# Performance work log

Measured on AMD Instinct MI355X. Metric: run time of the kernel, lower is better.

Reference implementation:

```python
import jax, jax.numpy as jnp
import numpy as np

N_NODES = 100000
N_EDGES = 1600000
EDGES_IN = 1
HID = 64
OUT = 64


def setup_inputs() -> dict:
    key = jax.random.key(0)
    ks = jax.random.split(key, 10)
    s = lambda fan_in: 1.0 / np.sqrt(fan_in)
    inp = {
        "edge_index": jax.random.randint(ks[0], (2, N_EDGES), 0, N_NODES, dtype=jnp.int64) if jax.config.jax_enable_x64 else jax.random.randint(ks[0], (2, N_EDGES), 0, N_NODES, dtype=jnp.int32),
        "edge_attr": jax.random.normal(ks[1], (N_EDGES, EDGES_IN), dtype=jnp.float32),
        # edge MLP: Linear(EDGES_IN->HID), SiLU, Linear(HID->HID), SiLU
        "W1": jax.random.uniform(ks[2], (EDGES_IN, HID), jnp.float32, -s(EDGES_IN), s(EDGES_IN)),
        "b1": jax.random.uniform(ks[3], (HID,), jnp.float32, -s(EDGES_IN), s(EDGES_IN)),
        "W2": jax.random.uniform(ks[4], (HID, HID), jnp.float32, -s(HID), s(HID)),
        "b2": jax.random.uniform(ks[5], (HID,), jnp.float32, -s(HID), s(HID)),
        # node MLP: Linear(HID->HID), SiLU, Linear(HID->OUT)
        "W3": jax.random.uniform(ks[6], (HID, HID), jnp.float32, -s(HID), s(HID)),
        "b3": jax.random.uniform(ks[7], (HID,), jnp.float32, -s(HID), s(HID)),
        "W4": jax.random.uniform(ks[8], (HID, OUT), jnp.float32, -s(HID), s(HID)),
        "b4": jax.random.uniform(ks[9], (OUT,), jnp.float32, -s(HID), s(HID)),
    }
    return inp


def reference(edge_index, edge_attr, W1, b1, W2, b2, W3, b3, W4, b4):
    silu = jax.nn.silu
    # edge model: [E, EDGES_IN] -> [E, HID]
    ef = silu(edge_attr @ W1 + b1)
    ef = silu(ef @ W2 + b2)
    # unsorted_segment_sum over source nodes (row): [E, HID] -> [N, HID]
    row = edge_index[0]
    agg = jax.ops.segment_sum(ef, row, num_segments=N_NODES)
    # node model: [N, HID] -> [N, OUT]
    h = silu(agg @ W3 + b3) @ W4 + b4
    return h
```

## Files before the change

kernel.cpp:

```cpp
#include <hip/hip_runtime.h>
#include <math.h>
#include <utility>

#define TN 4096
#define XMIN (-8.0f)
#define XMAX (8.0f)

#define GB1 256
#define MAXBK 4096
#define BKN 32
#define BKCAP 1024

typedef __attribute__((ext_vector_type(8))) short short8;
typedef __attribute__((ext_vector_type(4))) float f32x4;
typedef __attribute__((ext_vector_type(4))) int   int4v;
typedef __attribute__((ext_vector_type(4))) float f4v;

__device__ __forceinline__ float silu_f(float v) {
    return v / (1.0f + __expf(-v));
}

__device__ __forceinline__ unsigned short f2bf(float x) {
    unsigned u = __float_as_uint(x);
    return (unsigned short)((u + 0x7FFFu + ((u >> 16) & 1u)) >> 16);
}
__device__ __forceinline__ float bf2f(unsigned short h) {
    return __uint_as_float(((unsigned)h) << 16);
}

#define SPLIT8(w0,w1,w2,w3,w4,w5,w6,w7, H, L) { \
    unsigned short _h0=f2bf(w0),_h1=f2bf(w1),_h2=f2bf(w2),_h3=f2bf(w3), \
                   _h4=f2bf(w4),_h5=f2bf(w5),_h6=f2bf(w6),_h7=f2bf(w7); \
    H = (short8){(short)_h0,(short)_h1,(short)_h2,(short)_h3, \
                 (short)_h4,(short)_h5,(short)_h6,(short)_h7}; \
    L = (short8){(short)f2bf((w0)-bf2f(_h0)),(short)f2bf((w1)-bf2f(_h1)), \
                 (short)f2bf((w2)-bf2f(_h2)),(short)f2bf((w3)-bf2f(_h3)), \
                 (short)f2bf((w4)-bf2f(_h4)),(short)f2bf((w5)-bf2f(_h5)), \
                 (short)f2bf((w6)-bf2f(_h6)),(short)f2bf((w7)-bf2f(_h7))}; }

#define BFRAG(Wp, kc, nt, H, L) { \
    const float* _p = (Wp) + ((kc)*32 + quad*8)*64 + (nt)*16 + m; \
    SPLIT8(_p[0],_p[64],_p[128],_p[192],_p[256],_p[320],_p[384],_p[448], H, L) }

#define MFMA3(AH, AL, BH, BL, ACC) \
    ACC = __builtin_amdgcn_mfma_f32_16x16x32_bf16(AH, BH, ACC, 0, 0, 0); \
    ACC = __builtin_amdgcn_mfma_f32_16x16x32_bf16(AL, BH, ACC, 0, 0, 0); \
    ACC = __builtin_amdgcn_mfma_f32_16x16x32_bf16(AH, BL, ACC, 0, 0, 0);

__global__ void build_table_k(const float* __restrict__ W1, const float* __restrict__ b1,
                              const float* __restrict__ W2, const float* __restrict__ b2,
                              float* __restrict__ table2, int* __restrict__ cnt, int nbk) {
    int gid  = blockIdx.x * blockDim.x + threadIdx.x;
    if (gid < nbk) cnt[gid] = 0;
    int wave = gid >> 6;
    int lane = gid & 63;
    if (wave >= TN) return;
    const float step = (XMAX - XMIN) / (float)(TN - 1);
    float x  = XMIN + step * (float)wave;
    float h1 = silu_f(fmaf(x, W1[lane], b1[lane]));
    float acc = b2[lane];
#pragma unroll
    for (int k = 0; k < 64; ++k) {
        float h1k = __shfl(h1, k, 64);
        acc = fmaf(h1k, W2[k * 64 + lane], acc);
    }
    float val = silu_f(acc);
    table2[(size_t)wave * 128 + 2 * lane] = val;
    if (wave > 0)
        table2[(size_t)(wave - 1) * 128 + 2 * lane + 1] = val;
}

__global__ void pack_w_k(const float* __restrict__ W3, const float* __restrict__ W4,
                         short8* __restrict__ packW) {
    int t = threadIdx.x, lane = t & 63, wid = t >> 6;
    int m = lane & 15, quad = lane >> 4;
    for (int f = wid; f < 16; f += 4) {
        const float* Wp = (f < 8) ? W3 : W4;
        int kc = f & 1, nt = (f >> 1) & 3;
        short8 H, L;
        BFRAG(Wp, kc, nt, H, L)
        packW[(2 * f + 0) * 64 + lane] = H;
        packW[(2 * f + 1) * 64 + lane] = L;
    }
}

__global__ void bscatter_k(const int* __restrict__ row, const float* __restrict__ x,
                           int* __restrict__ cnt, unsigned int* __restrict__ packed,
                           int E, int nbk) {
    __shared__ int hist[MAXBK];
    int t = threadIdx.x;
    for (int e = t; e < nbk; e += 256) hist[e] = 0;
    __syncthreads();
    int E4 = E >> 2;
    for (int i4 = blockIdx.x * 256 + t; i4 < E4; i4 += 256 * GB1) {
        int4v r4 = ((const int4v*)row)[i4];
        atomicAdd(&hist[r4[0] >> 5], 1);
        atomicAdd(&hist[r4[1] >> 5], 1);
        atomicAdd(&hist[r4[2] >> 5], 1);
        atomicAdd(&hist[r4[3] >> 5], 1);
    }
    if (blockIdx.x == 0)
        for (int i = (E4 << 2) + t; i < E; i += 256)
            atomicAdd(&hist[row[i] >> 5], 1);
    __syncthreads();
    int shift = (int)(((long)blockIdx.x * nbk) >> 8);
    for (int k = t; k < nbk; k += 256) {
        int e = k + shift; if (e >= nbk) e -= nbk;
        int c = hist[e];
        hist[e] = c ? (e * BKCAP + atomicAdd(&cnt[e], c)) : 0;
    }
    __syncthreads();
    const float scale = (float)(TN - 1) / (XMAX - XMIN);
    for (int i4 = blockIdx.x * 256 + t; i4 < E4; i4 += 256 * GB1) {
        int4v r4 = ((const int4v*)row)[i4];
        f4v   x4 = ((const f4v*)x)[i4];
#pragma unroll
        for (int k = 0; k < 4; ++k) {
            int r = r4[k];
            float tt = fminf(fmaxf((x4[k] - XMIN) * scale, 0.f), (float)(TN - 1) - 0.001f);
            int   i0 = (int)tt;
            unsigned int q = min((unsigned int)((tt - (float)i0) * 8192.0f), 8191u);
            unsigned int pk = ((unsigned int)(r & 31) << 25) | ((unsigned int)i0 << 13) | q;
            int bk = r >> 5;
            int p = atomicAdd(&hist[bk], 1);
            if (p < (bk + 1) * BKCAP) packed[p] = pk;
        }
    }
    if (blockIdx.x == 0) {
        for (int i = (E4 << 2) + t; i < E; i += 256) {
            int r = row[i];
            float xv = x[i];
            float tt = fminf(fmaxf((xv - XMIN) * scale, 0.f), (float)(TN - 1) - 0.001f);
            int   i0 = (int)tt;
            unsigned int q = min((unsigned int)((tt - (float)i0) * 8192.0f), 8191u);
            unsigned int pk = ((unsigned int)(r & 31) << 25) | ((unsigned int)i0 << 13) | q;
            int bk = r >> 5;
            int p = atomicAdd(&hist[bk], 1);
            if (p < (bk + 1) * BKCAP) packed[p] = pk;
        }
    }
}

__global__ __launch_bounds__(256, 8)
void gather_k(const unsigned int* __restrict__ packed, const int* __restrict__ cntArr,
              const float* __restrict__ table2, float* __restrict__ aggOut, int N) {
    __shared__ __align__(16) unsigned int srt[BKCAP];
    __shared__ int hist[BKN + 1];
    __shared__ int curs[BKN];
    int t = threadIdx.x, lane = t & 63, wid = t >> 6;
    int b = blockIdx.x;

    int s   = b * BKCAP;
    int cnt = min(cntArr[b], BKCAP);

    if (t <= BKN) hist[t] = 0;
    __syncthreads();

    uint4 myq;
    int mybase = t << 2;
    int myrem = 0;
    if (mybase < cnt) {
        myq = *(const uint4*)&packed[s + mybase];
        myrem = cnt - mybase; if (myrem > 4) myrem = 4;
        if (myrem > 0) atomicAdd(&hist[myq.x >> 25], 1);
        if (myrem > 1) atomicAdd(&hist[myq.y >> 25], 1);
        if (myrem > 2) atomicAdd(&hist[myq.z >> 25], 1);
        if (myrem > 3) atomicAdd(&hist[myq.w >> 25], 1);
    }
    __syncthreads();

    if (wid == 0 && lane < BKN) {
        int c = hist[lane];
        int sc = c;
#pragma unroll
        for (int d = 1; d < BKN; d <<= 1) {
            int u = __shfl_up(sc, d, 64);
            if (lane >= d) sc += u;
        }
        hist[lane] = sc - c;  curs[lane] = sc - c;
        if (lane == BKN - 1) hist[BKN] = sc;
    }
    __syncthreads();

    if (myrem > 0) { int p = atomicAdd(&curs[myq.x >> 25], 1); srt[p] = myq.x; }
    if (myrem > 1) { int p = atomicAdd(&curs[myq.y >> 25], 1); srt[p] = myq.y; }
    if (myrem > 2) { int p = atomicAdd(&curs[myq.z >> 25], 1); srt[p] = myq.z; }
    if (myrem > 3) { int p = atomicAdd(&curs[myq.w >> 25], 1); srt[p] = myq.w; }
    __syncthreads();

    const float2* tb = (const float2*)table2;
#define EDGE_UV(sp, uv, f) \
    const float2* _rp = tb + (((sp >> 13) & 0xFFFu) << 6); \
    float2 uv = _rp[lane]; \
    float f = (float)(sp & 0x1FFFu) * (1.0f / 8192.0f);

    for (int nl = wid; nl < BKN; nl += 4) {
        int n = (b << 5) + nl;
        if (n >= N) break;
        int beg = hist[nl], dn = hist[nl + 1] - beg;
        float a0 = 0.f, a1 = 0.f, a2 = 0.f, a3 = 0.f;
        int j = 0;
        int head = (4 - (beg & 3)) & 3;
        if (head > dn) head = dn;
        for (; j < head; ++j) {
            unsigned sp0 = (unsigned)__builtin_amdgcn_readfirstlane(srt[beg + j]);
            EDGE_UV(sp0, uv0, f0)
            a0 = fmaf(f0, uv0.y - uv0.x, a0 + uv0.x);
        }
        for (; j + 8 <= dn; j += 8) {
            uint4 qa = *(const uint4*)&srt[beg + j];
            uint4 qb = *(const uint4*)&srt[beg + j + 4];
            unsigned sp0 = (unsigned)__builtin_amdgcn_readfirstlane(qa.x);
            unsigned sp1 = (unsigned)__builtin_amdgcn_readfirstlane(qa.y);
            unsigned sp2 = (unsigned)__builtin_amdgcn_readfirstlane(qa.z);
            unsigned sp3 = (unsigned)__builtin_amdgcn_readfirstlane(qa.w);
            unsigned sp4 = (unsigned)__builtin_amdgcn_readfirstlane(qb.x);
            unsigned sp5 = (unsigned)__builtin_amdgcn_readfirstlane(qb.y);
            unsigned sp6 = (unsigned)__builtin_amdgcn_readfirstlane(qb.z);
            unsigned sp7 = (unsigned)__builtin_amdgcn_readfirstlane(qb.w);
            { EDGE_UV(sp0, uv0, f0) a0 = fmaf(f0, uv0.y - uv0.x, a0 + uv0.x); }
            { EDGE_UV(sp1, uv1, f1) a1 = fmaf(f1, uv1.y - uv1.x, a1 + uv1.x); }
            { EDGE_UV(sp2, uv2, f2) a2 = fmaf(f2, uv2.y - uv2.x, a2 + uv2.x); }
            { EDGE_UV(sp3, uv3, f3) a3 = fmaf(f3, uv3.y - uv3.x, a3 + uv3.x); }
            { EDGE_UV(sp4, uv4, f4) a0 = fmaf(f4, uv4.y - uv4.x, a0 + uv4.x); }
            { EDGE_UV(sp5, uv5, f5) a1 = fmaf(f5, uv5.y - uv5.x, a1 + uv5.x); }
            { EDGE_UV(sp6, uv6, f6) a2 = fmaf(f6, uv6.y - uv6.x, a2 + uv6.x); }
            { EDGE_UV(sp7, uv7, f7) a3 = fmaf(f7, uv7.y - uv7.x, a3 + uv7.x); }
        }
        for (; j + 4 <= dn; j += 4) {
            uint4 q = *(const uint4*)&srt[beg + j];
            unsigned sp0 = (unsigned)__builtin_amdgcn_readfirstlane(q.x);
            unsigned sp1 = (unsigned)__builtin_amdgcn_readfirstlane(q.y);
            unsigned sp2 = (unsigned)__builtin_amdgcn_readfirstlane(q.z);
            unsigned sp3 = (unsigned)__builtin_amdgcn_readfirstlane(q.w);
            { EDGE_UV(sp0, uv0, f0) a0 = fmaf(f0, uv0.y - uv0.x, a0 + uv0.x); }
            { EDGE_UV(sp1, uv1, f1) a1 = fmaf(f1, uv1.y - uv1.x, a1 + uv1.x); }
            { EDGE_UV(sp2, uv2, f2) a2 = fmaf(f2, uv2.y - uv2.x, a2 + uv2.x); }
            { EDGE_UV(sp3, uv3, f3) a3 = fmaf(f3, uv3.y - uv3.x, a3 + uv3.x); }
        }
        for (; j < dn; ++j) {
            unsigned sp0 = (unsigned)__builtin_amdgcn_readfirstlane(srt[beg + j]);
            EDGE_UV(sp0, uv0, f0)
            a0 = fmaf(f0, uv0.y - uv0.x, a0 + uv0.x);
        }
        aggOut[(size_t)n * 64 + lane] = (a0 + a1) + (a2 + a3);
    }
#undef EDGE_UV
}

__global__ __launch_bounds__(256, 1)
void mlp_k(const short8* __restrict__ packW, const float* __restrict__ b3,
           const float* __restrict__ b4, float* __restrict__ h, int N, int ntiles) {
    __shared__ float gt[4][16 * 68];
    int t = threadIdx.x, lane = t & 63, wid = t >> 6;
    int m = lane & 15, quad = lane >> 4;

    const short8* pw = packW + lane;
#define LDW(s) pw[(s) * 64]
    short8 B3h00=LDW( 0), B3l00=LDW( 1), B3h01=LDW( 2), B3l01=LDW( 3);
    short8 B3h10=LDW( 4), B3l10=LDW( 5), B3h11=LDW( 6), B3l11=LDW( 7);
    short8 B3h20=LDW( 8), B3l20=LDW( 9), B3h21=LDW(10), B3l21=LDW(11);
    short8 B3h30=LDW(12), B3l30=LDW(13), B3h31=LDW(14), B3l31=LDW(15);
    short8 B4h00=LDW(16), B4l00=LDW(17), B4h01=LDW(18), B4l01=LDW(19);
    short8 B4h10=LDW(20), B4l10=LDW(21), B4h11=LDW(22), B4l11=LDW(23);
    short8 B4h20=LDW(24), B4l20=LDW(25), B4h21=LDW(26), B4l21=LDW(27);
    short8 B4h30=LDW(28), B4l30=LDW(29), B4h31=LDW(30), B4l31=LDW(31);
#undef LDW
    float c0 = b4[0*16 + m], c1 = b4[1*16 + m], c2 = b4[2*16 + m], c3 = b4[3*16 + m];
    float d0 = b3[0*16 + m], d1 = b3[1*16 + m], d2 = b3[2*16 + m], d3 = b3[3*16 + m];
    float* g = gt[wid];

    for (int tile = blockIdx.x; tile < ntiles; tile += gridDim.x) {
        long r0 = (long)tile * 64 + wid * 16;
        if (r0 >= N) continue;

        long ra = r0 + m; if (ra > N - 1) ra = N - 1;
        const float* ap = h + ra * 64 + quad * 8;
        float4 p0 = *(const float4*)(ap);       float4 p1 = *(const float4*)(ap + 4);
        float4 p2 = *(const float4*)(ap + 32);  float4 p3 = *(const float4*)(ap + 36);
        short8 Ah0, Al0, Ah1, Al1;
        SPLIT8(p0.x,p0.y,p0.z,p0.w,p1.x,p1.y,p1.z,p1.w, Ah0, Al0)
        SPLIT8(p2.x,p2.y,p2.z,p2.w,p3.x,p3.y,p3.z,p3.w, Ah1, Al1)

        f32x4 acc0 = {0.f,0.f,0.f,0.f}, acc1 = {0.f,0.f,0.f,0.f};
        f32x4 acc2 = {0.f,0.f,0.f,0.f}, acc3 = {0.f,0.f,0.f,0.f};
        MFMA3(Ah0, Al0, B3h00, B3l00, acc0)  MFMA3(Ah1, Al1, B3h01, B3l01, acc0)
        MFMA3(Ah0, Al0, B3h10, B3l10, acc1)  MFMA3(Ah1, Al1, B3h11, B3l11, acc1)
        MFMA3(Ah0, Al0, B3h20, B3l20, acc2)  MFMA3(Ah1, Al1, B3h21, B3l21, acc2)
        MFMA3(Ah0, Al0, B3h30, B3l30, acc3)  MFMA3(Ah1, Al1, B3h31, B3l31, acc3)

        g[(quad*4+0)*68 + 0*16 + m] = silu_f(acc0.x + d0);
        g[(quad*4+1)*68 + 0*16 + m] = silu_f(acc0.y + d0);
        g[(quad*4+2)*68 + 0*16 + m] = silu_f(acc0.z + d0);
        g[(quad*4+3)*68 + 0*16 + m] = silu_f(acc0.w + d0);
        g[(quad*4+0)*68 + 1*16 + m] = silu_f(acc1.x + d1);
        g[(quad*4+1)*68 + 1*16 + m] = silu_f(acc1.y + d1);
        g[(quad*4+2)*68 + 1*16 + m] = silu_f(acc1.z + d1);
        g[(quad*4+3)*68 + 1*16 + m] = silu_f(acc1.w + d1);
        g[(quad*4+0)*68 + 2*16 + m] = silu_f(acc2.x + d2);
        g[(quad*4+1)*68 + 2*16 + m] = silu_f(acc2.y + d2);
        g[(quad*4+2)*68 + 2*16 + m] = silu_f(acc2.z + d2);
        g[(quad*4+3)*68 + 2*16 + m] = silu_f(acc2.w + d2);
        g[(quad*4+0)*68 + 3*16 + m] = silu_f(acc3.x + d3);
        g[(quad*4+1)*68 + 3*16 + m] = silu_f(acc3.y + d3);
        g[(quad*4+2)*68 + 3*16 + m] = silu_f(acc3.z + d3);
        g[(quad*4+3)*68 + 3*16 + m] = silu_f(acc3.w + d3);

        const float* gp = g + m * 68 + quad * 8;
        float4 q0 = *(const float4*)(gp);       float4 q1 = *(const float4*)(gp + 4);
        float4 q2 = *(const float4*)(gp + 32);  float4 q3 = *(const float4*)(gp + 36);
        short8 Gh0, Gl0, Gh1, Gl1;
        SPLIT8(q0.x,q0.y,q0.z,q0.w,q1.x,q1.y,q1.z,q1.w, Gh0, Gl0)
        SPLIT8(q2.x,q2.y,q2.z,q2.w,q3.x,q3.y,q3.z,q3.w, Gh1, Gl1)

        f32x4 o0 = {0.f,0.f,0.f,0.f}, o1 = {0.f,0.f,0.f,0.f};
        f32x4 o2 = {0.f,0.f,0.f,0.f}, o3 = {0.f,0.f,0.f,0.f};
        MFMA3(Gh0, Gl0, B4h00, B4l00, o0)  MFMA3(Gh1, Gl1, B4h01, B4l01, o0)
        MFMA3(Gh0, Gl0, B4h10, B4l10, o1)  MFMA3(Gh1, Gl1, B4h11, B4l11, o1)
        MFMA3(Gh0, Gl0, B4h20, B4l20, o2)  MFMA3(Gh1, Gl1, B4h21, B4l21, o2)
        MFMA3(Gh0, Gl0, B4h30, B4l30, o3)  MFMA3(Gh1, Gl1, B4h31, B4l31, o3)

        long rw = r0 + quad * 4;
        if (rw + 0 < N) { float* o = h + (rw+0)*64;
            o[ 0+m]=o0.x+c0; o[16+m]=o1.x+c1; o[32+m]=o2.x+c2; o[48+m]=o3.x+c3; }
        if (rw + 1 < N) { float* o = h + (rw+1)*64;
            o[ 0+m]=o0.y+c0; o[16+m]=o1.y+c1; o[32+m]=o2.y+c2; o[48+m]=o3.y+c3; }
        if (rw + 2 < N) { float* o = h + (rw+2)*64;
            o[ 0+m]=o0.z+c0; o[16+m]=o1.z+c1; o[32+m]=o2.z+c2; o[48+m]=o3.z+c3; }
        if (rw + 3 < N) { float* o = h + (rw+3)*64;
            o[ 0+m]=o0.w+c0; o[16+m]=o1.w+c1; o[32+m]=o2.w+c2; o[48+m]=o3.w+c3; }
    }
}

__global__ void zero_k(float4* __restrict__ p, int n4) {
    int i = blockIdx.x * blockDim.x + threadIdx.x;
    int stride = gridDim.x * blockDim.x;
    float4 z = make_float4(0.f, 0.f, 0.f, 0.f);
    for (; i < n4; i += stride) p[i] = z;
}

__global__ void edge_k(const int* __restrict__ row, const float* __restrict__ xarr,
                       const float* __restrict__ table2, float* __restrict__ agg, int E) {
    int gid    = blockIdx.x * blockDim.x + threadIdx.x;
    int lane   = gid & 63;
    int wave   = gid >> 6;
    int nwaves = (gridDim.x * blockDim.x) >> 6;
    const float scale = (float)(TN - 1) / (XMAX - XMIN);
    const float2* tab = (const float2*)table2 + lane;
    for (int e = wave; e < E; e += nwaves) {
        float x = xarr[e];
        int   r = row[e];
        float t = fminf(fmaxf((x - XMIN) * scale, 0.0f), (float)(TN - 1) - 0.001f);
        int   i0 = (int)t;
        float f  = t - (float)i0;
        float2 uv = tab[i0 << 6];
        atomicAdd(agg + (size_t)r * 64 + lane, fmaf(f, uv.y - uv.x, uv.x));
    }
}

extern "C" void kernel_launch(void* const* d_in, const int* in_sizes, int n_in,
                              void* d_out, int out_size, void* d_ws, size_t ws_size,
                              hipStream_t stream) {
    const int*   edge_index = (const int*)  d_in[0];
    const float* edge_attr  = (const float*)d_in[1];
    const float* W1 = (const float*)d_in[2];
    const float* b1 = (const float*)d_in[3];
    const float* W2 = (const float*)d_in[4];
    const float* b2 = (const float*)d_in[5];
    const float* W3 = (const float*)d_in[6];
    const float* b3 = (const float*)d_in[7];
    const float* W4 = (const float*)d_in[8];
    const float* b4 = (const float*)d_in[9];

    float* out = (float*)d_out;
    const int E   = in_sizes[1];
    const int N   = out_size / 64;
    const int nbk = (N + BKN - 1) / BKN;
    const int nmb = (N + 63) / 64;

    char* ws = (char*)d_ws;
    size_t off = 0;
    auto carve = [&](size_t bytes) { size_t r = off; off = (off + bytes + 255) & ~(size_t)255; return r; };
    size_t tableOff = carve((size_t)TN * 128 * 4);
    size_t packWOff = carve((size_t)32 * 64 * 16);
    size_t cntOff   = carve((size_t)nbk * 4);
    size_t pkOff    = carve((size_t)nbk * BKCAP * 4);
    bool fits = (off <= ws_size) && (nbk <= MAXBK);

    float*  table2 = (float*)(ws + tableOff);
    short8* packW  = (short8*)(ws + packWOff);
    int*    cnt    = (int*)(ws + cntOff);

    build_table_k<<<TN / 4, 256, 0, stream>>>(W1, b1, W2, b2, table2, cnt,
                                              fits ? nbk : 0);
    pack_w_k<<<1, 256, 0, stream>>>(W3, W4, packW);

    if (fits) {
        unsigned int* packed = (unsigned int*)(ws + pkOff);

        bscatter_k<<<GB1, 256, 0, stream>>>(edge_index, edge_attr, cnt, packed, E, nbk);
        gather_k  <<<nbk, 256, 0, stream>>>(packed, cnt, table2, out, N);
        mlp_k     <<<512, 256, 0, stream>>>(packW, b3, b4, out, N, nmb);
    } else {
        zero_k<<<4096, 256, 0, stream>>>((float4*)out, (N * 64) / 4);
        edge_k<<<8192, 256, 0, stream>>>(edge_index, edge_attr, table2, out, E);
        mlp_k <<<512, 256, 0, stream>>>(packW, b3, b4, out, N, nmb);
    }
}
```

Baseline: 191.6 us.

## Fold weight packing into table kernel, unroll gather by 16, retune grid sizes

Merges the single-block W3/W4 packing kernel into the table-build kernel as an extra block, removing one kernel launch. Adds a 16-edge unrolled gather loop so more table loads are in flight per wave. Halves the bucket-scatter grid (adjusting the shift stagger to match) and doubles the MLP grid. The larger unroll raises register pressure, and fewer scatter blocks means each block handles more edges.

```diff
diff --git a/kernel.cpp b/kernel.cpp
--- a/kernel.cpp
+++ b/kernel.cpp
@@ -6,7 +6,7 @@
 #define XMIN (-8.0f)
 #define XMAX (8.0f)
 
-#define GB1 256
+#define GB1 128
 #define MAXBK 4096
 #define BKN 32
 #define BKCAP 1024
@@ -49,9 +49,24 @@
 
 __global__ void build_table_k(const float* __restrict__ W1, const float* __restrict__ b1,
                               const float* __restrict__ W2, const float* __restrict__ b2,
+                              const float* __restrict__ W3, const float* __restrict__ W4,
+                              short8* __restrict__ packW,
                               float* __restrict__ table2, int* __restrict__ cnt, int nbk) {
     int gid  = blockIdx.x * blockDim.x + threadIdx.x;
     if (gid < nbk) cnt[gid] = 0;
+    if (blockIdx.x == TN / 4) {
+        int t = threadIdx.x, lane = t & 63, wid = t >> 6;
+        int m = lane & 15, quad = lane >> 4;
+        for (int f = wid; f < 16; f += 4) {
+            const float* Wp = (f < 8) ? W3 : W4;
+            int kc = f & 1, nt = (f >> 1) & 3;
+            short8 H, L;
+            BFRAG(Wp, kc, nt, H, L)
+            packW[(2 * f + 0) * 64 + lane] = H;
+            packW[(2 * f + 1) * 64 + lane] = L;
+        }
+        return;
+    }
     int wave = gid >> 6;
     int lane = gid & 63;
     if (wave >= TN) return;
@@ -70,20 +85,6 @@
         table2[(size_t)(wave - 1) * 128 + 2 * lane + 1] = val;
 }
 
-__global__ void pack_w_k(const float* __restrict__ W3, const float* __restrict__ W4,
-                         short8* __restrict__ packW) {
-    int t = threadIdx.x, lane = t & 63, wid = t >> 6;
-    int m = lane & 15, quad = lane >> 4;
-    for (int f = wid; f < 16; f += 4) {
-        const float* Wp = (f < 8) ? W3 : W4;
-        int kc = f & 1, nt = (f >> 1) & 3;
-        short8 H, L;
-        BFRAG(Wp, kc, nt, H, L)
-        packW[(2 * f + 0) * 64 + lane] = H;
-        packW[(2 * f + 1) * 64 + lane] = L;
-    }
-}
-
 __global__ void bscatter_k(const int* __restrict__ row, const float* __restrict__ x,
                            int* __restrict__ cnt, unsigned int* __restrict__ packed,
                            int E, int nbk) {
@@ -103,7 +104,7 @@
         for (int i = (E4 << 2) + t; i < E; i += 256)
             atomicAdd(&hist[row[i] >> 5], 1);
     __syncthreads();
-    int shift = (int)(((long)blockIdx.x * nbk) >> 8);
+    int shift = (int)(((long)blockIdx.x * nbk) >> 7);
     for (int k = t; k < nbk; k += 256) {
         int e = k + shift; if (e >= nbk) e -= nbk;
         int c = hist[e];
@@ -206,6 +207,44 @@
             unsigned sp0 = (unsigned)__builtin_amdgcn_readfirstlane(srt[beg + j]);
             EDGE_UV(sp0, uv0, f0)
             a0 = fmaf(f0, uv0.y - uv0.x, a0 + uv0.x);
+        }
+        for (; j + 16 <= dn; j += 16) {
+            uint4 qa = *(const uint4*)&srt[beg + j];
+            uint4 qb = *(const uint4*)&srt[beg + j + 4];
+            uint4 qc = *(const uint4*)&srt[beg + j + 8];
+            uint4 qd = *(const uint4*)&srt[beg + j + 12];
+            unsigned sp0 = (unsigned)__builtin_amdgcn_readfirstlane(qa.x);
+            unsigned sp1 = (unsigned)__builtin_amdgcn_readfirstlane(qa.y);
+            unsigned sp2 = (unsigned)__builtin_amdgcn_readfirstlane(qa.z);
+            unsigned sp3 = (unsigned)__builtin_amdgcn_readfirstlane(qa.w);
+            unsigned sp4 = (unsigned)__builtin_amdgcn_readfirstlane(qb.x);
+            unsigned sp5 = (unsigned)__builtin_amdgcn_readfirstlane(qb.y);
+            unsigned sp6 = (unsigned)__builtin_amdgcn_readfirstlane(qb.z);
+            unsigned sp7 = (unsigned)__builtin_amdgcn_readfirstlane(qb.w);
+            unsigned sp8 = (unsigned)__builtin_amdgcn_readfirstlane(qc.x);
+            unsigned sp9 = (unsigned)__builtin_amdgcn_readfirstlane(qc.y);
+            unsigned spA = (unsigned)__builtin_amdgcn_readfirstlane(qc.z);
+            unsigned spB = (unsigned)__builtin_amdgcn_readfirstlane(qc.w);
+            unsigned spC = (unsigned)__builtin_amdgcn_readfirstlane(qd.x);
+            unsigned spD = (unsigned)__builtin_amdgcn_readfirstlane(qd.y);
+            unsigned spE = (unsigned)__builtin_amdgcn_readfirstlane(qd.z);
+            unsigned spF = (unsigned)__builtin_amdgcn_readfirstlane(qd.w);
+            { EDGE_UV(sp0, uv0, f0) a0 = fmaf(f0, uv0.y - uv0.x, a0 + uv0.x); }
+            { EDGE_UV(sp1, uv1, f1) a1 = fmaf(f1, uv1.y - uv1.x, a1 + uv1.x); }
+            { EDGE_UV(sp2, uv2, f2) a2 = fmaf(f2, uv2.y - uv2.x, a2 + uv2.x); }
+            { EDGE_UV(sp3, uv3, f3) a3 = fmaf(f3, uv3.y - uv3.x, a3 + uv3.x); }
+            { EDGE_UV(sp4, uv4, f4) a0 = fmaf(f4, uv4.y - uv4.x, a0 + uv4.x); }
+            { EDGE_UV(sp5, uv5, f5) a1 = fmaf(f5, uv5.y - uv5.x, a1 + uv5.x); }
+            { EDGE_UV(sp6, uv6, f6) a2 = fmaf(f6, uv6.y - uv6.x, a2 + uv6.x); }
+            { EDGE_UV(sp7, uv7, f7) a3 = fmaf(f7, uv7.y - uv7.x, a3 + uv7.x); }
+            { EDGE_UV(sp8, uv8, f8) a0 = fmaf(f8, uv8.y - uv8.x, a0 + uv8.x); }
+            { EDGE_UV(sp9, uv9, f9) a1 = fmaf(f9, uv9.y - uv9.x, a1 + uv9.x); }
+            { EDGE_UV(spA, uvA, fA) a2 = fmaf(fA, uvA.y - uvA.x, a2 + uvA.x); }
+            { EDGE_UV(spB, uvB, fB) a3 = fmaf(fB, uvB.y - uvB.x, a3 + uvB.x); }
+            { EDGE_UV(spC, uvC, fC) a0 = fmaf(fC, uvC.y - uvC.x, a0 + uvC.x); }
+            { EDGE_UV(spD, uvD, fD) a1 = fmaf(fD, uvD.y - uvD.x, a1 + uvD.x); }
+            { EDGE_UV(spE, uvE, fE) a2 = fmaf(fE, uvE.y - uvE.x, a2 + uvE.x); }
+            { EDGE_UV(spF, uvF, fF) a3 = fmaf(fF, uvF.y - uvF.x, a3 + uvF.x); }
         }
         for (; j + 8 <= dn; j += 8) {
             uint4 qa = *(const uint4*)&srt[beg + j];
@@ -391,19 +430,18 @@
     short8* packW  = (short8*)(ws + packWOff);
     int*    cnt    = (int*)(ws + cntOff);
 
-    build_table_k<<<TN / 4, 256, 0, stream>>>(W1, b1, W2, b2, table2, cnt,
-                                              fits ? nbk : 0);
-    pack_w_k<<<1, 256, 0, stream>>>(W3, W4, packW);
+    build_table_k<<<TN / 4 + 1, 256, 0, stream>>>(W1, b1, W2, b2, W3, W4, packW,
+                                                  table2, cnt, fits ? nbk : 0);
 
     if (fits) {
         unsigned int* packed = (unsigned int*)(ws + pkOff);
 
         bscatter_k<<<GB1, 256, 0, stream>>>(edge_index, edge_attr, cnt, packed, E, nbk);
         gather_k  <<<nbk, 256, 0, stream>>>(packed, cnt, table2, out, N);
-        mlp_k     <<<512, 256, 0, stream>>>(packW, b3, b4, out, N, nmb);
+        mlp_k     <<<1024, 256, 0, stream>>>(packW, b3, b4, out, N, nmb);
     } else {
         zero_k<<<4096, 256, 0, stream>>>((float4*)out, (N * 64) / 4);
         edge_k<<<8192, 256, 0, stream>>>(edge_index, edge_attr, table2, out, E);
-        mlp_k <<<512, 256, 0, stream>>>(packW, b3, b4, out, N, nmb);
-    }
-}
+        mlp_k <<<1024, 256, 0, stream>>>(packW, b3, b4, out, N, nmb);
+    }
+}
```

Measured after the change: 194.3 us. About the same (+1.4%).
